# Kernel optimization log

Measured on AMD Instinct MI355X. Metric: run time of the kernel, lower is better.

## Reference

```python
import jax, jax.numpy as jnp
import numpy as np

V, E, H, B, T1, T2 = 32000, 300, 300, 64, 48, 48


def _lstm_last(x, Wih, Whh, bih, bhh):
    # x: [T, B, in]; returns final hidden state h_T: [B, H] (PyTorch gate order i,f,g,o)
    h0 = jnp.zeros((x.shape[1], Whh.shape[1]), x.dtype)
    def step(carry, xt):
        h, c = carry
        g = xt @ Wih.T + h @ Whh.T + bih + bhh
        i, f, gc, o = jnp.split(g, 4, axis=-1)
        c = jax.nn.sigmoid(f) * c + jax.nn.sigmoid(i) * jnp.tanh(gc)
        h = jax.nn.sigmoid(o) * jnp.tanh(c)
        return (h, c), None
    (h, _), _ = jax.lax.scan(step, (h0, h0), x)
    return h


def _bilstm_last(x, pf, pr):
    hf = _lstm_last(x, *pf)
    hr = _lstm_last(x[::-1], *pr)
    # faithful quirk: original reverses projr[0] along dim 0 == BATCH dim
    return jnp.concatenate([hf, hr[::-1]], axis=1)  # [B, 2H]


def _forward(x1, x2, x1_mask, x2_mask,
             emb, eW, eU, ebi, ebh, rW, rU, rbi, rbh,
             dW, dU, dbi, dbh, sW, sU, sbi, sbh,
             f1w, f1b, f2w, f2b, fow, fob):
    emb1 = emb[x1]  # [T1,B,E]
    emb2 = emb[x2]
    # encoder outputs final hidden [B,2H], broadcast over time by mask multiply (faithful quirk)
    ctx1 = _bilstm_last(emb1, (eW, eU, ebi, ebh), (rW, rU, rbi, rbh))[None] * x1_mask[:, :, None]  # [T1,B,2H]
    ctx2 = _bilstm_last(emb2, (eW, eU, ebi, ebh), (rW, rU, rbi, rbh))[None] * x2_mask[:, :, None]  # [T2,B,2H]
    c1 = ctx1.transpose(1, 0, 2)  # [B,T1,2H]
    c2 = ctx2.transpose(1, 0, 2)  # [B,T2,2H]
    # scores[b,i,j] = max_d c1[b,i,d]*c2[b,j,d]  (vectorized form of the O(T1*T2) python loop)
    scores = jnp.max(c1[:, :, None, :] * c2[:, None, :, :], axis=-1)  # [B,T1,T2]
    m1 = x1_mask.T  # [B,T1]
    m2 = x2_mask.T  # [B,T2]
    # masked softmax over hypothesis axis (axis=2)
    ea = jnp.exp(scores - jnp.max(scores, axis=2, keepdims=True)) * m2[:, None, :]
    alpha = ea / jnp.sum(ea, axis=2, keepdims=True)  # [B,T1,T2]
    # faithful quirk: MAX (not sum) pooling of attention-weighted hypothesis
    a_tilde = jnp.max(alpha[:, :, :, None] * c2[:, None, :, :], axis=2)  # [B,T1,2H]
    # masked softmax over premise axis (axis=1)
    eb = jnp.exp(scores - jnp.max(scores, axis=1, keepdims=True)) * m1[:, :, None]
    beta = eb / jnp.sum(eb, axis=1, keepdims=True)  # [B,T1,T2]
    b_tilde = jnp.einsum('bij,bid->bjd', beta, c1)  # [B,T2,2H]
    ctx1_ = a_tilde.transpose(1, 0, 2)  # [T1,B,2H]
    ctx2_ = b_tilde.transpose(1, 0, 2)  # [T2,B,2H]
    inp1 = jnp.concatenate([ctx1, ctx1_, ctx1 * ctx1_, ctx1 - ctx1_], axis=2)  # [T1,B,8H]
    inp2 = jnp.concatenate([ctx2, ctx2_, ctx2 * ctx2_, ctx2 - ctx2_], axis=2)
    h1 = jax.nn.relu(inp1 @ f1w.T + f1b)
    h2 = jax.nn.relu(inp2 @ f1w.T + f1b)
    ctx3 = _bilstm_last(h1, (dW, dU, dbi, dbh), (sW, sU, sbi, sbh))  # [B,2H]
    ctx4 = _bilstm_last(h2, (dW, dU, dbi, dbh), (sW, sU, sbi, sbh))  # [B,2H]
    w3 = ctx3[None] * x1_mask[:, :, None]  # [T1,B,2H]
    w4 = ctx4[None] * x2_mask[:, :, None]  # [T2,B,2H]
    logit = jnp.concatenate([
        w3.sum(0) / x1_mask.sum(0)[:, None], w3.max(0),
        w4.sum(0) / x2_mask.sum(0)[:, None], w4.max(0)], axis=1)  # [B,8H]
    logit = jnp.tanh(logit @ f2w.T + f2b)
    return logit @ fow.T + fob  # [B,3]


def setup_inputs() -> dict:
    key = jax.random.key(0)
    ks = jax.random.split(key, 32)
    s = 0.05
    n = lambda k, shape: jax.random.normal(k, shape, jnp.float32) * s
    d = {
        'x1': jax.random.randint(ks[0], (T1, B), 0, V, dtype=jnp.int32),
        'x1_mask': jnp.ones((T1, B), jnp.float32),
        'x2': jax.random.randint(ks[1], (T2, B), 0, V, dtype=jnp.int32),
        'x2_mask': jnp.ones((T2, B), jnp.float32),
        'l': T1,
        'embed_table': n(ks[2], (V, E)),
        'enc_Wih': n(ks[3], (4 * H, E)), 'enc_Whh': n(ks[4], (4 * H, H)),
        'enc_bih': n(ks[5], (4 * H,)), 'enc_bhh': n(ks[6], (4 * H,)),
        'encr_Wih': n(ks[7], (4 * H, E)), 'encr_Whh': n(ks[8], (4 * H, H)),
        'encr_bih': n(ks[9], (4 * H,)), 'encr_bhh': n(ks[10], (4 * H,)),
        'dec_Wih': n(ks[11], (4 * H, H)), 'dec_Whh': n(ks[12], (4 * H, H)),
        'dec_bih': n(ks[13], (4 * H,)), 'dec_bhh': n(ks[14], (4 * H,)),
        'decr_Wih': n(ks[15], (4 * H, H)), 'decr_Whh': n(ks[16], (4 * H, H)),
        'decr_bih': n(ks[17], (4 * H,)), 'decr_bhh': n(ks[18], (4 * H,)),
        'fc1_w': n(ks[19], (H, 8 * H)), 'fc1_b': n(ks[20], (H,)),
        'fc2_w': n(ks[21], (H, 8 * H)), 'fc2_b': n(ks[22], (H,)),
        'fco_w': n(ks[23], (3, H)), 'fco_b': n(ks[24], (3,)),
    }
    return d


def reference(x1, x1_mask, x2, x2_mask, l, embed_table,
              enc_Wih, enc_Whh, enc_bih, enc_bhh,
              encr_Wih, encr_Whh, encr_bih, encr_bhh,
              dec_Wih, dec_Whh, dec_bih, dec_bhh,
              decr_Wih, decr_Whh, decr_bih, decr_bhh,
              fc1_w, fc1_b, fc2_w, fc2_b, fco_w, fco_b):
    del l  # unused in original forward
    return _forward(x1, x2, x1_mask, x2_mask, embed_table,
                    enc_Wih, enc_Whh, enc_bih, enc_bhh,
                    encr_Wih, encr_Whh, encr_bih, encr_bhh,
                    dec_Wih, dec_Whh, dec_bih, dec_bhh,
                    decr_Wih, decr_Whh, decr_bih, decr_bhh,
                    fc1_w, fc1_b, fc2_w, fc2_b, fco_w, fco_b)
```

## Files before the change

kernel.cpp:

```cpp
#include <hip/hip_runtime.h>
#include <math.h>

typedef unsigned short u16;
typedef unsigned int u32;
typedef unsigned long long u64;
typedef __attribute__((ext_vector_type(8))) __bf16 bf16x8;
typedef __attribute__((ext_vector_type(4))) float f32x4;
typedef __attribute__((ext_vector_type(4))) _Float16 f16x4;

#define MR   6144
#define KP1  320
#define NPG  1280
#define NG   1200
#define WSEG 409600
#define UPSEG 409600
#define GT_H 163840

#define OFF_ABF    0UL
#define OFF_WBF    3932160UL
#define OFF_WCF    10485760UL
#define OFF_BIAS   12645760UL
#define OFF_GF     12664960UL
#define OFF_GR     28393600UL
#define OFF_HB     44122240UL
#define OFF_ENC    44286080UL
#define OFF_VB     44593280UL
#define OFF_CO     45822080UL
#define OFF_ATT    46436480UL
#define OFF_PT     46473344UL
#define OFF_LG     47087744UL
#define OFF_UP     47164544UL

#define HX_BYTES   655360UL

__device__ __forceinline__ float sigf(float x) { return 1.0f / (1.0f + expf(-x)); }
__device__ __forceinline__ float fsig(float x) { return 1.0f / (1.0f + __expf(-x)); }
__device__ __forceinline__ float ftanh(float x) { return 1.0f - 2.0f / (__expf(2.0f * x) + 1.0f); }

__device__ __forceinline__ u16 f2bf(float x) {
    union { float f; u32 u; } v; v.f = x;
    u32 r = v.u + 0x7fffu + ((v.u >> 16) & 1u);
    return (u16)(r >> 16);
}
__device__ __forceinline__ float bf2f(u16 x) {
    union { u32 u; float f; } v; v.u = ((u32)x) << 16; return v.f;
}

__device__ __forceinline__ void gld_lds16(const u16* g, u16* l) {
    __builtin_amdgcn_global_load_lds(
        (const __attribute__((address_space(1))) unsigned int*)g,
        (__attribute__((address_space(3))) unsigned int*)l, 16, 0, 0);
}

__global__ __launch_bounds__(256) void gather_bf(const int* __restrict__ x1,
                                                 const int* __restrict__ x2,
                                                 const float* __restrict__ emb,
                                                 u16* __restrict__ abf) {
    int idx = blockIdx.x * 256 + threadIdx.x;
    if (idx >= MR * KP1) return;
    int r = idx / KP1, k = idx % KP1;
    float v = 0.0f;
    if (k < 300) {
        int t = r >> 7, bc = r & 127;
        int tok = (bc < 64) ? x1[t * 64 + bc] : x2[t * 64 + bc - 64];
        v = emb[tok * 300 + k];
    }
    abf[idx] = f2bf(v);
}

__global__ __launch_bounds__(256) void wconv8_k(const float* __restrict__ w0, const float* __restrict__ w1,
                                                const float* __restrict__ w2, const float* __restrict__ w3,
                                                const float* __restrict__ w4, const float* __restrict__ w5,
                                                const float* __restrict__ w6, const float* __restrict__ w7,
                                                u16* __restrict__ out) {
    int idx = blockIdx.x * 256 + threadIdx.x;
    if (idx >= 8 * NPG * KP1) return;
    int s = idx / (NPG * KP1), rem = idx % (NPG * KP1);
    int r = rem / KP1, k = rem % KP1;
    const float* w = (s == 0) ? w0 : (s == 1) ? w1 : (s == 2) ? w2 : (s == 3) ? w3
                   : (s == 4) ? w4 : (s == 5) ? w5 : (s == 6) ? w6 : w7;
    float v = 0.0f;
    if (r < NG && k < 300) {
        int j = r >> 2, g = r & 3;
        v = w[(g * 300 + j) * 300 + k];
    }
    out[idx] = f2bf(v);
}

__global__ __launch_bounds__(256) void uperm_k(const u16* __restrict__ WU,
                                               u16* __restrict__ UP) {
    int idx = blockIdx.x * 256 + threadIdx.x;
    if (idx >= 4 * UPSEG) return;
    int seg = idx / UPSEG, pos = idx % UPSEG;
    int T = pos / 5120, kt = (pos / 512) % 10, l = (pos >> 3) & 63, e = pos & 7;
    int n = T * 16 + (l & 15);
    int k = kt * 32 + (l >> 4) * 8 + e;
    UP[idx] = WU[(size_t)seg * WSEG + (size_t)n * KP1 + k];
}

__global__ __launch_bounds__(256) void bconv_k(const float* __restrict__ b0i, const float* __restrict__ b0h,
                                               const float* __restrict__ b1i, const float* __restrict__ b1h,
                                               const float* __restrict__ b2i, const float* __restrict__ b2h,
                                               const float* __restrict__ b3i, const float* __restrict__ b3h,
                                               float* __restrict__ out) {
    int idx = blockIdx.x * 256 + threadIdx.x;
    if (idx >= 4 * NG) return;
    int s = idx / NG, n = idx % NG;
    int j = n >> 2, g = n & 3;
    int src = g * 300 + j;
    const float* bi = (s == 0) ? b0i : (s == 1) ? b1i : (s == 2) ? b2i : b3i;
    const float* bh = (s == 0) ? b0h : (s == 1) ? b1h : (s == 2) ? b2h : b3h;
    out[idx] = bi[src] + bh[src];
}

__global__ __launch_bounds__(256) void wcat_k(const float* __restrict__ f1w,
                                              float* __restrict__ wc) {
    int idx = blockIdx.x * 256 + threadIdx.x;
    if (idx >= 300 * 1800) return;
    int n = idx / 1800, k = idx % 1800;
    int nk = n * 2400 + k;
    float v;
    if (k < 600)       v = f1w[nk] + f1w[nk + 1800];
    else if (k < 1200) v = f1w[nk] - f1w[nk + 1200];
    else               v = f1w[nk];
    wc[idx] = v;
}

__global__ __launch_bounds__(256) void gemm_bt(const u16* __restrict__ A,
                                               const u16* __restrict__ B,
                                               const float* __restrict__ bias,
                                               _Float16* __restrict__ Gh) {
    __shared__ __align__(16) u16 smA[128 * 32];
    __shared__ __align__(16) u16 smB[128 * 32];
    int m0 = blockIdx.x * 128, n0 = blockIdx.y * 128;
    int tid = threadIdx.x, ln = tid & 63;
    int wm = (tid >> 6) & 1, wn = tid >> 7;
    int lrow = ln & 15, lq = ln >> 4;
    f32x4 acc[4][4] = {};
    for (int k0 = 0; k0 < KP1; k0 += 32) {
#pragma unroll
        for (int p = 0; p < 2; p++) {
            int e = (p * 256 + tid) * 8;
            int r = e >> 5, kk = e & 31;
            gld_lds16(A + (size_t)(m0 + r) * KP1 + k0 + kk, smA + e);
            gld_lds16(B + (size_t)(n0 + r) * KP1 + k0 + kk, smB + e);
        }
        __syncthreads();
        bf16x8 av[4], bv[4];
#pragma unroll
        for (int i = 0; i < 4; i++) {
            av[i] = *(const bf16x8*)&smA[(wm * 64 + i * 16 + lrow) * 32 + lq * 8];
            bv[i] = *(const bf16x8*)&smB[(wn * 64 + i * 16 + lrow) * 32 + lq * 8];
        }
#pragma unroll
        for (int i = 0; i < 4; i++)
#pragma unroll
            for (int j = 0; j < 4; j++)
                acc[i][j] = __builtin_amdgcn_mfma_f32_16x16x32_bf16(av[i], bv[j], acc[i][j], 0, 0, 0);
        __syncthreads();
    }
    size_t tb = (size_t)blockIdx.x * GT_H + (size_t)blockIdx.y * 16384
              + (size_t)wm * 8192 + (size_t)wn * 2048 + (size_t)ln * 4;
#pragma unroll
    for (int i = 0; i < 4; i++)
#pragma unroll
        for (int j = 0; j < 4; j++) {
            int n = n0 + wn * 64 + j * 16 + lrow;
            f16x4 v;
            if (n < NG) {
                float bb = bias[n];
#pragma unroll
                for (int r = 0; r < 4; r++) v[r] = (_Float16)(acc[i][j][r] + bb);
            } else {
                v = (f16x4)0;
            }
            *(f16x4*)(Gh + tb + (size_t)(i >> 1) * 4096 + (size_t)(((i & 1) * 4 + j)) * 256) = v;
        }
}

__global__ __launch_bounds__(256, 1) void lstm_sync(const _Float16* __restrict__ Gf,
                                                    const _Float16* __restrict__ Gr,
                                                    const u16* __restrict__ Upf,
                                                    const u16* __restrict__ Upr,
                                                    u64* __restrict__ hx,
                                                    u16* __restrict__ hb) {
    int nt = blockIdx.x, dir = blockIdx.y, half = blockIdx.z;
    const _Float16* G = dir ? Gr : Gf;
    const u16* Up = dir ? Upr : Upf;

    int tid = threadIdx.x, ln = tid & 63, w = tid >> 6;
    int wm = w & 1, wn = w >> 1;
    int lrow = ln & 15, lq = ln >> 4;

    __shared__ __align__(16) u16 Ulds[80 * 512];
    __shared__ __align__(16) u32 Hst[64 * 160];
    __shared__ float P[64][132];

    for (int p = 0; p < 20; p++) {
        int e = (p * 256 + tid) * 8;
        gld_lds16(Up + (size_t)nt * 40960 + e, Ulds + e);
    }
    __syncthreads();

    u32* HOw = (u32*)hb;

    int jp = tid & 15, bg = tid >> 4;
    float c[4][2];
#pragma unroll
    for (int q = 0; q < 4; q++) { c[q][0] = 0.0f; c[q][1] = 0.0f; }

    const _Float16* Gs = G + (size_t)nt * 16384 + (size_t)half * 8192
                       + (size_t)wm * 4096 + (size_t)wn * 2048 + (size_t)ln * 4;
    f16x4 gpre[8];
    {
        int ttg = dir ? 47 : 0;
        const _Float16* Gt = Gs + (size_t)ttg * GT_H;
#pragma unroll
        for (int f = 0; f < 8; f++) gpre[f] = *(const f16x4*)(Gt + (size_t)f * 256);
    }

    for (int t = 0; t < 48; t++) {
        {
            const u64* slab = hx + ((size_t)(t & 1) * 2 + dir) * 20480 + (size_t)half * 10240;
            u32 want = (u32)t;
            u32 hv[40];
            for (;;) {
                bool ok = true;
#pragma unroll
                for (int q = 0; q < 40; q++) {
                    u64 x = __hip_atomic_load(slab + q * 256 + tid,
                                              __ATOMIC_RELAXED, __HIP_MEMORY_SCOPE_AGENT);
                    hv[q] = (u32)x;
                    ok &= ((u32)(x >> 32) == want);
                }
                if (ok) break;
                __builtin_amdgcn_s_sleep(1);
            }
#pragma unroll
            for (int q = 0; q < 40; q++) {
                int idx = q * 256 + tid;
                int row = idx / 160, cc = idx - row * 160;
                Hst[row * 160 + (cc ^ ((row & 7) << 2))] = hv[q];
            }
        }
        __syncthreads();

        f32x4 acc[2][4];
#pragma unroll
        for (int i = 0; i < 2; i++)
#pragma unroll
            for (int j = 0; j < 4; j++) {
                f32x4 a;
#pragma unroll
                for (int r = 0; r < 4; r++) a[r] = (float)gpre[i * 4 + j][r];
                acc[i][j] = a;
            }

#pragma unroll
        for (int kt = 0; kt < 10; kt++) {
            bf16x8 av[2], bv[4];
#pragma unroll
            for (int i = 0; i < 2; i++) {
                int row = wm * 32 + i * 16 + lrow;
                int cc = (kt * 16 + lq * 4) ^ ((row & 7) << 2);
                av[i] = *(const bf16x8*)&Hst[row * 160 + cc];
            }
#pragma unroll
            for (int j = 0; j < 4; j++)
                bv[j] = *(const bf16x8*)&Ulds[((size_t)(wn * 4 + j) * 10 + kt) * 512 + ln * 8];
#pragma unroll
            for (int i = 0; i < 2; i++)
#pragma unroll
                for (int j = 0; j < 4; j++)
                    acc[i][j] = __builtin_amdgcn_mfma_f32_16x16x32_bf16(av[i], bv[j], acc[i][j], 0, 0, 0);
        }

#pragma unroll
        for (int i = 0; i < 2; i++)
#pragma unroll
            for (int j = 0; j < 4; j++) {
                int col = wn * 64 + j * 16 + lrow;
#pragma unroll
                for (int r = 0; r < 4; r++)
                    P[wm * 32 + i * 16 + lq * 4 + r][col] = acc[i][j][r];
            }
        __syncthreads();

        if (t < 47) {
            int ttg = dir ? 46 - t : t + 1;
            const _Float16* Gt = Gs + (size_t)ttg * GT_H;
#pragma unroll
            for (int f = 0; f < 8; f++) gpre[f] = *(const f16x4*)(Gt + (size_t)f * 256);
        }

        {
            u64* hxo = hx + ((size_t)((t + 1) & 1) * 2 + dir) * 20480;
            u64 tagb = ((u64)(u32)(t + 1)) << 32;
#pragma unroll
            for (int q = 0; q < 4; q++) {
                int bc = bg * 4 + q;
                f32x4 g0 = *(const f32x4*)&P[bc][8 * jp];
                f32x4 g1 = *(const f32x4*)&P[bc][8 * jp + 4];
                float cn0 = fsig(g0[1]) * c[q][0] + fsig(g0[0]) * ftanh(g0[2]);
                float hn0 = fsig(g0[3]) * ftanh(cn0);
                float cn1 = fsig(g1[1]) * c[q][1] + fsig(g1[0]) * ftanh(g1[2]);
                float hn1 = fsig(g1[3]) * ftanh(cn1);
                c[q][0] = cn0; c[q][1] = cn1;
                u32 pk = (u32)f2bf(hn0) | ((u32)f2bf(hn1) << 16);
                int bcg = half * 64 + bc;
                size_t oi = (size_t)bcg * 160 + nt * 16 + jp;
                if (t < 47)
                    __hip_atomic_store(hxo + oi, (u64)pk | tagb,
                                       __ATOMIC_RELAXED, __HIP_MEMORY_SCOPE_AGENT);
                else
                    HOw[(size_t)dir * 20480 + oi] = pk;
            }
        }
        __syncthreads();
    }
}

__global__ __launch_bounds__(256) void enc_k(const u16* __restrict__ hF,
                                             const u16* __restrict__ hR,
                                             float* __restrict__ enc) {
    int idx = blockIdx.x * 256 + threadIdx.x;
    if (idx >= 128 * 600) return;
    int bc = idx / 600, d = idx % 600;
    int seq = bc >> 6, b = bc & 63;
    enc[idx] = (d < 300) ? bf2f(hF[bc * KP1 + d])
                         : bf2f(hR[(seq * 64 + 63 - b) * KP1 + d - 300]);
}

__global__ __launch_bounds__(256) void vbuf_k(const float* __restrict__ enc,
                                              float* __restrict__ V) {
    int idx = blockIdx.x * 256 + threadIdx.x;
    if (idx >= 64 * 600) return;
    int b = idx / 600, d = idx % 600;
    float e1 = enc[b * 600 + d], e2 = enc[(64 + b) * 600 + d];
    float p = fmaxf(e2, 0.0f), nn = fminf(e2, 0.0f);
    V[0 * 38400 + idx] = e1;
    V[1 * 38400 + idx] = p;
    V[2 * 38400 + idx] = nn;
    V[3 * 38400 + idx] = e1 * p;
    V[4 * 38400 + idx] = e1 * nn;
    V[5 * 38400 + idx] = e2;
    V[6 * 38400 + idx] = e1;
    V[7 * 38400 + idx] = e1 * e2;
}

__global__ __launch_bounds__(256) void attn_lite(const float* __restrict__ enc,
                                                 const float* __restrict__ x1m,
                                                 const float* __restrict__ x2m,
                                                 float* __restrict__ AMX,
                                                 float* __restrict__ AMN,
                                                 float* __restrict__ SS) {
    int b = blockIdx.x, tid = threadIdx.x;
    __shared__ float sc[48][49];
    __shared__ float rmx[4], rmn[4];
    __shared__ float MxMn[2];
    float mx = -3.4e38f, mn = 3.4e38f;
    for (int d = tid; d < 600; d += 256) {
        float p = enc[b * 600 + d] * enc[(64 + b) * 600 + d];
        mx = fmaxf(mx, p); mn = fminf(mn, p);
    }
    for (int off = 32; off; off >>= 1) {
        mx = fmaxf(mx, __shfl_down(mx, off));
        mn = fminf(mn, __shfl_down(mn, off));
    }
    if ((tid & 63) == 0) { rmx[tid >> 6] = mx; rmn[tid >> 6] = mn; }
    __syncthreads();
    if (tid == 0) {
        MxMn[0] = fmaxf(fmaxf(rmx[0], rmx[1]), fmaxf(rmx[2], rmx[3]));
        MxMn[1] = fminf(fminf(rmn[0], rmn[1]), fminf(rmn[2], rmn[3]));
    }
    __syncthreads();
    float Mx = MxMn[0], Mn = MxMn[1];
    for (int idx = tid; idx < 2304; idx += 256) {
        int i = idx / 48, j = idx % 48;
        float q = x1m[i * 64 + b] * x2m[j * 64 + b];
        sc[i][j] = (q > 0.0f) ? q * Mx : ((q < 0.0f) ? q * Mn : 0.0f);
    }
    __syncthreads();
    if (tid < 48) {
        int i = tid;
        float m = -3.4e38f;
        for (int j = 0; j < 48; j++) m = fmaxf(m, sc[i][j]);
        float sum = 0.0f;
        for (int j = 0; j < 48; j++) sum += expf(sc[i][j] - m) * x2m[j * 64 + b];
        float wmax = -3.4e38f, wmin = 3.4e38f;
        for (int j = 0; j < 48; j++) {
            float w = expf(sc[i][j] - m) * x2m[j * 64 + b] * x2m[j * 64 + b];
            wmax = fmaxf(wmax, w); wmin = fminf(wmin, w);
        }
        AMX[i * 64 + b] = wmax / sum;
        AMN[i * 64 + b] = wmin / sum;
    } else if (tid >= 64 && tid < 112) {
        int j = tid - 64;
        float m = -3.4e38f;
        for (int i = 0; i < 48; i++) m = fmaxf(m, sc[i][j]);
        float sum = 0.0f, sm = 0.0f;
        for (int i = 0; i < 48; i++) {
            float e = expf(sc[i][j] - m) * x1m[i * 64 + b];
            sum += e; sm += e * x1m[i * 64 + b];
        }
        SS[j * 64 + b] = sm / sum;
    }
}

__global__ __launch_bounds__(256) void coeff_gemm(const float* __restrict__ V,
                                                  const float* __restrict__ Wc,
                                                  float* __restrict__ CO) {
    __shared__ float As[16][64];
    __shared__ float Ws[16][64];
    int s = blockIdx.y;
    const int offs[8] = {0, 600, 600, 1200, 1200, 0, 600, 1200};
    int koff = offs[s];
    const float* A = V + (size_t)s * 38400;
    float* C = CO + (size_t)s * 19200;
    int n0 = blockIdx.x * 64;
    int tid = threadIdx.x;
    int lrow = tid >> 2;
    int lk4 = (tid & 3) << 2;
    int tm = (tid & 15) << 2;
    int tn = (tid >> 4) << 2;
    int nW = n0 + lrow;
    float acc[4][4] = {};
    for (int k0 = 0; k0 < 600; k0 += 16) {
        __syncthreads();
#pragma unroll
        for (int q = 0; q < 4; q++) {
            int k = k0 + lk4 + q;
            As[lk4 + q][lrow] = (k < 600) ? A[lrow * 600 + k] : 0.0f;
            Ws[lk4 + q][lrow] = (k < 600 && nW < 300) ? Wc[(size_t)nW * 1800 + koff + k] : 0.0f;
        }
        __syncthreads();
#pragma unroll
        for (int kk = 0; kk < 16; kk++) {
            float a0 = As[kk][tm], a1 = As[kk][tm + 1], a2 = As[kk][tm + 2], a3 = As[kk][tm + 3];
            float w0 = Ws[kk][tn], w1 = Ws[kk][tn + 1], w2 = Ws[kk][tn + 2], w3 = Ws[kk][tn + 3];
            acc[0][0] += a0 * w0; acc[0][1] += a0 * w1; acc[0][2] += a0 * w2; acc[0][3] += a0 * w3;
            acc[1][0] += a1 * w0; acc[1][1] += a1 * w1; acc[1][2] += a1 * w2; acc[1][3] += a1 * w3;
            acc[2][0] += a2 * w0; acc[2][1] += a2 * w1; acc[2][2] += a2 * w2; acc[2][3] += a2 * w3;
            acc[3][0] += a3 * w0; acc[3][1] += a3 * w1; acc[3][2] += a3 * w2; acc[3][3] += a3 * w3;
        }
    }
#pragma unroll
    for (int ii = 0; ii < 4; ii++) {
        int m = tm + ii;
#pragma unroll
        for (int jn = 0; jn < 4; jn++) {
            int n = n0 + tn + jn;
            if (n < 300) C[m * 300 + n] = acc[ii][jn];
        }
    }
}

__global__ __launch_bounds__(320) void combine_k(const float* __restrict__ CO,
                                                 const float* __restrict__ f1b,
                                                 const float* __restrict__ x1m,
                                                 const float* __restrict__ x2m,
                                                 const float* __restrict__ AMX,
                                                 const float* __restrict__ AMN,
                                                 const float* __restrict__ SS,
                                                 u16* __restrict__ OUT) {
    int r = blockIdx.x;
    int t = r >> 7, bc = r & 127;
    int seq = bc >> 6, b = bc & 63;
    int n = threadIdx.x;
    if (n >= 300) return;
    int bn = b * 300 + n;
    float pre;
    if (seq == 0) {
        float m1 = x1m[t * 64 + b], am = AMX[t * 64 + b], an = AMN[t * 64 + b];
        pre = m1 * CO[bn] + am * CO[19200 + bn] + an * CO[2 * 19200 + bn]
            + m1 * am * CO[3 * 19200 + bn] + m1 * an * CO[4 * 19200 + bn] + f1b[n];
    } else {
        float m2 = x2m[t * 64 + b], sv = SS[t * 64 + b];
        pre = m2 * CO[5 * 19200 + bn] + sv * CO[6 * 19200 + bn]
            + m2 * sv * CO[7 * 19200 + bn] + f1b[n];
    }
    OUT[(size_t)r * KP1 + n] = f2bf(fmaxf(pre, 0.0f));
}

__global__ __launch_bounds__(256) void pool_k(const float* __restrict__ dctx,
                                              const float* __restrict__ x1m,
                                              const float* __restrict__ x2m,
                                              float* __restrict__ pooledT) {
    int idx = blockIdx.x * 256 + threadIdx.x;
    if (idx >= 64 * 2400) return;
    int b = idx / 2400, col = idx % 2400;
    int sec = col / 600, d = col % 600;
    const float* msk = (sec < 2) ? x1m : x2m;
    float v = dctx[((sec < 2 ? 0 : 64) + b) * 600 + d];
    float out;
    if ((sec & 1) == 0) {
        float s = 0, sm = 0;
        for (int t = 0; t < 48; t++) { float mv = msk[t * 64 + b]; s += v * mv; sm += mv; }
        out = s / sm;
    } else {
        float m = -3.4e38f;
        for (int t = 0; t < 48; t++) m = fmaxf(m, v * msk[t * 64 + b]);
        out = m;
    }
    pooledT[col * 64 + b] = out;
}

__global__ __launch_bounds__(256) void fc2_k2(const float* __restrict__ pooledT,
                                              const float* __restrict__ f2w,
                                              const float* __restrict__ f2b,
                                              float* __restrict__ logit) {
    __shared__ float wl[2400];
    __shared__ float red[256];
    int n = blockIdx.x;
    for (int i = threadIdx.x; i < 2400; i += 256) wl[i] = f2w[n * 2400 + i];
    __syncthreads();
    int b = threadIdx.x & 63, kc = threadIdx.x >> 6;
    float acc = 0.0f;
    int k0 = kc * 600;
    for (int kk = 0; kk < 600; kk++) acc += pooledT[(k0 + kk) * 64 + b] * wl[k0 + kk];
    red[threadIdx.x] = acc;
    __syncthreads();
    if (threadIdx.x < 64) {
        float s = red[b] + red[64 + b] + red[128 + b] + red[192 + b];
        logit[b * 300 + n] = tanhf(s + f2b[n]);
    }
}

__global__ __launch_bounds__(64) void out_k2(const float* __restrict__ logit,
                                             const float* __restrict__ fow,
                                             const float* __restrict__ fob,
                                             float* __restrict__ out) {
    int b = blockIdx.x, tid = threadIdx.x;
    float p0 = 0, p1 = 0, p2 = 0;
    for (int k = tid; k < 300; k += 64) {
        float l = logit[b * 300 + k];
        p0 += l * fow[k]; p1 += l * fow[300 + k]; p2 += l * fow[600 + k];
    }
    for (int off = 32; off; off >>= 1) {
        p0 += __shfl_down(p0, off);
        p1 += __shfl_down(p1, off);
        p2 += __shfl_down(p2, off);
    }
    if (tid == 0) {
        out[b * 3 + 0] = p0 + fob[0];
        out[b * 3 + 1] = p1 + fob[1];
        out[b * 3 + 2] = p2 + fob[2];
    }
}

extern "C" void kernel_launch(void* const* d_in, const int* in_sizes, int n_in,
                              void* d_out, int out_size, void* d_ws, size_t ws_size,
                              hipStream_t stream) {
    (void)in_sizes; (void)n_in; (void)out_size; (void)ws_size;
    const int*   x1  = (const int*)d_in[0];
    const float* x1m = (const float*)d_in[1];
    const int*   x2  = (const int*)d_in[2];
    const float* x2m = (const float*)d_in[3];
    const float* emb = (const float*)d_in[5];
    const float* eW  = (const float*)d_in[6];
    const float* eU  = (const float*)d_in[7];
    const float* ebi = (const float*)d_in[8];
    const float* ebh = (const float*)d_in[9];
    const float* rW  = (const float*)d_in[10];
    const float* rU  = (const float*)d_in[11];
    const float* rbi = (const float*)d_in[12];
    const float* rbh = (const float*)d_in[13];
    const float* dW  = (const float*)d_in[14];
    const float* dU  = (const float*)d_in[15];
    const float* dbi = (const float*)d_in[16];
    const float* dbh = (const float*)d_in[17];
    const float* sW  = (const float*)d_in[18];
    const float* sU  = (const float*)d_in[19];
    const float* sbi = (const float*)d_in[20];
    const float* sbh = (const float*)d_in[21];
    const float* f1w = (const float*)d_in[22];
    const float* f1b = (const float*)d_in[23];
    const float* f2w = (const float*)d_in[24];
    const float* f2b = (const float*)d_in[25];
    const float* fow = (const float*)d_in[26];
    const float* fob = (const float*)d_in[27];

    char* wsb = (char*)d_ws;
    u16*       ABF  = (u16*)(wsb + OFF_ABF);
    u16*       WBF  = (u16*)(wsb + OFF_WBF);
    float*     WCF  = (float*)(wsb + OFF_WCF);
    float*     BIAS = (float*)(wsb + OFF_BIAS);
    _Float16*  GFh  = (_Float16*)(wsb + OFF_GF);
    _Float16*  GRh  = (_Float16*)(wsb + OFF_GR);
    u16*       HB   = (u16*)(wsb + OFF_HB);
    float*     ENC  = (float*)(wsb + OFF_ENC);
    float*     VB   = (float*)(wsb + OFF_VB);
    float*     CO   = (float*)(wsb + OFF_CO);
    float*     AMX  = (float*)(wsb + OFF_ATT);
    float*     AMN  = AMX + 3072;
    float*     SS   = AMX + 6144;
    float*     PT   = (float*)(wsb + OFF_PT);
    float*     LG   = (float*)(wsb + OFF_LG);
    u16*       UP   = (u16*)(wsb + OFF_UP);
    u64*       HX64 = (u64*)(wsb + OFF_ABF);

    u16* HF0 = HB;
    u16* HR0 = HB + 40960;

    gather_bf<<<dim3((MR * KP1 + 255) / 256), 256, 0, stream>>>(x1, x2, emb, ABF);
    wconv8_k<<<dim3((8 * NPG * KP1 + 255) / 256), 256, 0, stream>>>(eW, rW, dW, sW, eU, rU, dU, sU, WBF);
    uperm_k<<<dim3((4 * UPSEG + 255) / 256), 256, 0, stream>>>(WBF + 4 * WSEG, UP);
    bconv_k<<<dim3((4 * NG + 255) / 256), 256, 0, stream>>>(ebi, ebh, rbi, rbh, dbi, dbh, sbi, sbh, BIAS);
    wcat_k<<<dim3((300 * 1800 + 255) / 256), 256, 0, stream>>>(f1w, WCF);

    gemm_bt<<<dim3(48, 10), 256, 0, stream>>>(ABF, WBF,        BIAS,      GFh);
    gemm_bt<<<dim3(48, 10), 256, 0, stream>>>(ABF, WBF + WSEG, BIAS + NG, GRh);
    hipMemsetAsync(wsb + OFF_ABF, 0, HX_BYTES, stream);
    lstm_sync<<<dim3(10, 2, 2), 256, 0, stream>>>(GFh, GRh, UP, UP + UPSEG, HX64, HB);

    enc_k<<<dim3((128 * 600 + 255) / 256), 256, 0, stream>>>(HF0, HR0, ENC);
    vbuf_k<<<dim3((64 * 600 + 255) / 256), 256, 0, stream>>>(ENC, VB);
    attn_lite<<<dim3(64), 256, 0, stream>>>(ENC, x1m, x2m, AMX, AMN, SS);
    coeff_gemm<<<dim3(5, 8), 256, 0, stream>>>(VB, WCF, CO);
    combine_k<<<dim3(6144), 320, 0, stream>>>(CO, f1b, x1m, x2m, AMX, AMN, SS, ABF);

    gemm_bt<<<dim3(48, 10), 256, 0, stream>>>(ABF, WBF + 2 * WSEG, BIAS + 2 * NG, GFh);
    gemm_bt<<<dim3(48, 10), 256, 0, stream>>>(ABF, WBF + 3 * WSEG, BIAS + 3 * NG, GRh);
    hipMemsetAsync(wsb + OFF_ABF, 0, HX_BYTES, stream);
    lstm_sync<<<dim3(10, 2, 2), 256, 0, stream>>>(GFh, GRh, UP + 2 * UPSEG, UP + 3 * UPSEG, HX64, HB);

    enc_k<<<dim3((128 * 600 + 255) / 256), 256, 0, stream>>>(HF0, HR0, ENC);
    pool_k<<<dim3((64 * 2400 + 255) / 256), 256, 0, stream>>>(ENC, x1m, x2m, PT);
    fc2_k2<<<dim3(300), 256, 0, stream>>>(PT, f2w, f2b, LG);
    out_k2<<<dim3(64), 64, 0, stream>>>(LG, fow, fob, (float*)d_out);
}
```

Before: 889.7 us.

## Fuse prep kernels, batch paired GEMMs, and relax LSTM polling and sync

The five weight/embedding preparation kernels become one block-partitioned prep kernel, and the recurrent weights are permuted straight from fp32 instead of through an intermediate bf16 copy. The forward and reverse input-projection GEMMs are merged into a single launch using a z grid dimension. In the persistent LSTM loop, the spin-wait now re-polls only the slab entries that have not yet arrived, the trailing __syncthreads is dropped, and the next-step gate prefetch moves after the hidden-state publish. This cuts launch count and per-step latency, but dropping the barrier relies on the later barrier inside the loop to keep shared-memory reuse safe.

```diff
diff --git a/kernel.cpp b/kernel.cpp
--- a/kernel.cpp
+++ b/kernel.cpp
@@ -33,7 +33,6 @@
 
 #define HX_BYTES   655360UL
 
-__device__ __forceinline__ float sigf(float x) { return 1.0f / (1.0f + expf(-x)); }
 __device__ __forceinline__ float fsig(float x) { return 1.0f / (1.0f + __expf(-x)); }
 __device__ __forceinline__ float ftanh(float x) { return 1.0f - 2.0f / (__expf(2.0f * x) + 1.0f); }
 
@@ -52,86 +51,94 @@
         (__attribute__((address_space(3))) unsigned int*)l, 16, 0, 0);
 }
 
-__global__ __launch_bounds__(256) void gather_bf(const int* __restrict__ x1,
-                                                 const int* __restrict__ x2,
-                                                 const float* __restrict__ emb,
-                                                 u16* __restrict__ abf) {
-    int idx = blockIdx.x * 256 + threadIdx.x;
-    if (idx >= MR * KP1) return;
-    int r = idx / KP1, k = idx % KP1;
-    float v = 0.0f;
-    if (k < 300) {
-        int t = r >> 7, bc = r & 127;
-        int tok = (bc < 64) ? x1[t * 64 + bc] : x2[t * 64 + bc - 64];
-        v = emb[tok * 300 + k];
-    }
-    abf[idx] = f2bf(v);
-}
-
-__global__ __launch_bounds__(256) void wconv8_k(const float* __restrict__ w0, const float* __restrict__ w1,
-                                                const float* __restrict__ w2, const float* __restrict__ w3,
-                                                const float* __restrict__ w4, const float* __restrict__ w5,
-                                                const float* __restrict__ w6, const float* __restrict__ w7,
-                                                u16* __restrict__ out) {
-    int idx = blockIdx.x * 256 + threadIdx.x;
-    if (idx >= 8 * NPG * KP1) return;
-    int s = idx / (NPG * KP1), rem = idx % (NPG * KP1);
-    int r = rem / KP1, k = rem % KP1;
-    const float* w = (s == 0) ? w0 : (s == 1) ? w1 : (s == 2) ? w2 : (s == 3) ? w3
-                   : (s == 4) ? w4 : (s == 5) ? w5 : (s == 6) ? w6 : w7;
-    float v = 0.0f;
-    if (r < NG && k < 300) {
-        int j = r >> 2, g = r & 3;
-        v = w[(g * 300 + j) * 300 + k];
-    }
-    out[idx] = f2bf(v);
-}
-
-__global__ __launch_bounds__(256) void uperm_k(const u16* __restrict__ WU,
-                                               u16* __restrict__ UP) {
-    int idx = blockIdx.x * 256 + threadIdx.x;
-    if (idx >= 4 * UPSEG) return;
-    int seg = idx / UPSEG, pos = idx % UPSEG;
-    int T = pos / 5120, kt = (pos / 512) % 10, l = (pos >> 3) & 63, e = pos & 7;
-    int n = T * 16 + (l & 15);
-    int k = kt * 32 + (l >> 4) * 8 + e;
-    UP[idx] = WU[(size_t)seg * WSEG + (size_t)n * KP1 + k];
-}
-
-__global__ __launch_bounds__(256) void bconv_k(const float* __restrict__ b0i, const float* __restrict__ b0h,
-                                               const float* __restrict__ b1i, const float* __restrict__ b1h,
-                                               const float* __restrict__ b2i, const float* __restrict__ b2h,
-                                               const float* __restrict__ b3i, const float* __restrict__ b3h,
-                                               float* __restrict__ out) {
-    int idx = blockIdx.x * 256 + threadIdx.x;
-    if (idx >= 4 * NG) return;
-    int s = idx / NG, n = idx % NG;
-    int j = n >> 2, g = n & 3;
-    int src = g * 300 + j;
-    const float* bi = (s == 0) ? b0i : (s == 1) ? b1i : (s == 2) ? b2i : b3i;
-    const float* bh = (s == 0) ? b0h : (s == 1) ? b1h : (s == 2) ? b2h : b3h;
-    out[idx] = bi[src] + bh[src];
-}
-
-__global__ __launch_bounds__(256) void wcat_k(const float* __restrict__ f1w,
-                                              float* __restrict__ wc) {
-    int idx = blockIdx.x * 256 + threadIdx.x;
-    if (idx >= 300 * 1800) return;
-    int n = idx / 1800, k = idx % 1800;
-    int nk = n * 2400 + k;
-    float v;
-    if (k < 600)       v = f1w[nk] + f1w[nk + 1800];
-    else if (k < 1200) v = f1w[nk] - f1w[nk + 1200];
-    else               v = f1w[nk];
-    wc[idx] = v;
+#define PREP_B0 7680
+#define PREP_B1 14080
+#define PREP_B2 20480
+#define PREP_B3 20499
+#define PREP_B4 22609
+__global__ __launch_bounds__(256) void prep_k(
+    const int* __restrict__ x1, const int* __restrict__ x2, const float* __restrict__ emb,
+    const float* __restrict__ w0, const float* __restrict__ w1,
+    const float* __restrict__ w2, const float* __restrict__ w3,
+    const float* __restrict__ u0, const float* __restrict__ u1,
+    const float* __restrict__ u2, const float* __restrict__ u3,
+    const float* __restrict__ b0i, const float* __restrict__ b0h,
+    const float* __restrict__ b1i, const float* __restrict__ b1h,
+    const float* __restrict__ b2i, const float* __restrict__ b2h,
+    const float* __restrict__ b3i, const float* __restrict__ b3h,
+    const float* __restrict__ f1w,
+    u16* __restrict__ abf, u16* __restrict__ wbf, u16* __restrict__ up,
+    float* __restrict__ bias, float* __restrict__ wc) {
+    int bid = blockIdx.x;
+    if (bid < PREP_B0) {
+        int idx = bid * 256 + threadIdx.x;
+        int r = idx / KP1, k = idx % KP1;
+        float v = 0.0f;
+        if (k < 300) {
+            int t = r >> 7, bc = r & 127;
+            int tok = (bc < 64) ? x1[t * 64 + bc] : x2[t * 64 + bc - 64];
+            v = emb[tok * 300 + k];
+        }
+        abf[idx] = f2bf(v);
+    } else if (bid < PREP_B1) {
+        int idx = (bid - PREP_B0) * 256 + threadIdx.x;
+        int s = idx / (NPG * KP1), rem = idx % (NPG * KP1);
+        int r = rem / KP1, k = rem % KP1;
+        const float* w = (s == 0) ? w0 : (s == 1) ? w1 : (s == 2) ? w2 : w3;
+        float v = 0.0f;
+        if (r < NG && k < 300) {
+            int j = r >> 2, g = r & 3;
+            v = w[(g * 300 + j) * 300 + k];
+        }
+        wbf[idx] = f2bf(v);
+    } else if (bid < PREP_B2) {
+        int idx = (bid - PREP_B1) * 256 + threadIdx.x;
+        int seg = idx / UPSEG, pos = idx % UPSEG;
+        int T = pos / 5120, kt = (pos / 512) % 10, l = (pos >> 3) & 63, e = pos & 7;
+        int n = T * 16 + (l & 15);
+        int k = kt * 32 + (l >> 4) * 8 + e;
+        const float* us = (seg == 0) ? u0 : (seg == 1) ? u1 : (seg == 2) ? u2 : u3;
+        float v = 0.0f;
+        if (n < NG && k < 300) {
+            int j = n >> 2, g = n & 3;
+            v = us[(g * 300 + j) * 300 + k];
+        }
+        up[idx] = f2bf(v);
+    } else if (bid < PREP_B3) {
+        int idx = (bid - PREP_B2) * 256 + threadIdx.x;
+        if (idx < 4 * NG) {
+            int s = idx / NG, n = idx % NG;
+            int j = n >> 2, g = n & 3;
+            int src = g * 300 + j;
+            const float* bi = (s == 0) ? b0i : (s == 1) ? b1i : (s == 2) ? b2i : b3i;
+            const float* bh = (s == 0) ? b0h : (s == 1) ? b1h : (s == 2) ? b2h : b3h;
+            bias[idx] = bi[src] + bh[src];
+        }
+    } else {
+        int idx = (bid - PREP_B3) * 256 + threadIdx.x;
+        if (idx < 300 * 1800) {
+            int n = idx / 1800, k = idx % 1800;
+            int nk = n * 2400 + k;
+            float v;
+            if (k < 600)       v = f1w[nk] + f1w[nk + 1800];
+            else if (k < 1200) v = f1w[nk] - f1w[nk + 1200];
+            else               v = f1w[nk];
+            wc[idx] = v;
+        }
+    }
 }
 
 __global__ __launch_bounds__(256) void gemm_bt(const u16* __restrict__ A,
-                                               const u16* __restrict__ B,
-                                               const float* __restrict__ bias,
-                                               _Float16* __restrict__ Gh) {
+                                               const u16* __restrict__ Wb,
+                                               const float* __restrict__ biasb,
+                                               _Float16* __restrict__ G0,
+                                               _Float16* __restrict__ G1) {
     __shared__ __align__(16) u16 smA[128 * 32];
     __shared__ __align__(16) u16 smB[128 * 32];
+    int sidx = blockIdx.z;
+    const u16* B = Wb + (size_t)sidx * WSEG;
+    const float* bias = biasb + sidx * NG;
+    _Float16* Gh = sidx ? G1 : G0;
     int m0 = blockIdx.x * 128, n0 = blockIdx.y * 128;
     int tid = threadIdx.x, ln = tid & 63;
     int wm = (tid >> 6) & 1, wn = tid >> 7;
@@ -224,17 +231,24 @@
             const u64* slab = hx + ((size_t)(t & 1) * 2 + dir) * 20480 + (size_t)half * 10240;
             u32 want = (u32)t;
             u32 hv[40];
-            for (;;) {
-                bool ok = true;
+            u64 miss = 0;
+#pragma unroll
+            for (int q = 0; q < 40; q++) {
+                u64 x = __hip_atomic_load(slab + q * 256 + tid,
+                                          __ATOMIC_RELAXED, __HIP_MEMORY_SCOPE_AGENT);
+                hv[q] = (u32)x;
+                miss |= ((u64)((u32)(x >> 32) != want)) << q;
+            }
+            while (miss) {
+                __builtin_amdgcn_s_sleep(1);
 #pragma unroll
                 for (int q = 0; q < 40; q++) {
-                    u64 x = __hip_atomic_load(slab + q * 256 + tid,
-                                              __ATOMIC_RELAXED, __HIP_MEMORY_SCOPE_AGENT);
-                    hv[q] = (u32)x;
-                    ok &= ((u32)(x >> 32) == want);
+                    if (miss & (1ull << q)) {
+                        u64 x = __hip_atomic_load(slab + q * 256 + tid,
+                                                  __ATOMIC_RELAXED, __HIP_MEMORY_SCOPE_AGENT);
+                        if ((u32)(x >> 32) == want) { hv[q] = (u32)x; miss &= ~(1ull << q); }
+                    }
                 }
-                if (ok) break;
-                __builtin_amdgcn_s_sleep(1);
             }
 #pragma unroll
             for (int q = 0; q < 40; q++) {
@@ -285,13 +299,6 @@
                     P[wm * 32 + i * 16 + lq * 4 + r][col] = acc[i][j][r];
             }
         __syncthreads();
-
-        if (t < 47) {
-            int ttg = dir ? 46 - t : t + 1;
-            const _Float16* Gt = Gs + (size_t)ttg * GT_H;
-#pragma unroll
-            for (int f = 0; f < 8; f++) gpre[f] = *(const f16x4*)(Gt + (size_t)f * 256);
-        }
 
         {
             u64* hxo = hx + ((size_t)((t + 1) & 1) * 2 + dir) * 20480;
@@ -316,7 +323,13 @@
                     HOw[(size_t)dir * 20480 + oi] = pk;
             }
         }
-        __syncthreads();
+
+        if (t < 47) {
+            int ttg = dir ? 46 - t : t + 1;
+            const _Float16* Gt = Gs + (size_t)ttg * GT_H;
+#pragma unroll
+            for (int f = 0; f < 8; f++) gpre[f] = *(const f16x4*)(Gt + (size_t)f * 256);
+        }
     }
 }
 
@@ -602,14 +615,12 @@
     u16* HF0 = HB;
     u16* HR0 = HB + 40960;
 
-    gather_bf<<<dim3((MR * KP1 + 255) / 256), 256, 0, stream>>>(x1, x2, emb, ABF);
-    wconv8_k<<<dim3((8 * NPG * KP1 + 255) / 256), 256, 0, stream>>>(eW, rW, dW, sW, eU, rU, dU, sU, WBF);
-    uperm_k<<<dim3((4 * UPSEG + 255) / 256), 256, 0, stream>>>(WBF + 4 * WSEG, UP);
-    bconv_k<<<dim3((4 * NG + 255) / 256), 256, 0, stream>>>(ebi, ebh, rbi, rbh, dbi, dbh, sbi, sbh, BIAS);
-    wcat_k<<<dim3((300 * 1800 + 255) / 256), 256, 0, stream>>>(f1w, WCF);
-
-    gemm_bt<<<dim3(48, 10), 256, 0, stream>>>(ABF, WBF,        BIAS,      GFh);
-    gemm_bt<<<dim3(48, 10), 256, 0, stream>>>(ABF, WBF + WSEG, BIAS + NG, GRh);
+    prep_k<<<dim3(PREP_B4), 256, 0, stream>>>(
+        x1, x2, emb, eW, rW, dW, sW, eU, rU, dU, sU,
+        ebi, ebh, rbi, rbh, dbi, dbh, sbi, sbh, f1w,
+        ABF, WBF, UP, BIAS, WCF);
+
+    gemm_bt<<<dim3(48, 10, 2), 256, 0, stream>>>(ABF, WBF, BIAS, GFh, GRh);
     hipMemsetAsync(wsb + OFF_ABF, 0, HX_BYTES, stream);
     lstm_sync<<<dim3(10, 2, 2), 256, 0, stream>>>(GFh, GRh, UP, UP + UPSEG, HX64, HB);
 
@@ -619,8 +630,7 @@
     coeff_gemm<<<dim3(5, 8), 256, 0, stream>>>(VB, WCF, CO);
     combine_k<<<dim3(6144), 320, 0, stream>>>(CO, f1b, x1m, x2m, AMX, AMN, SS, ABF);
 
-    gemm_bt<<<dim3(48, 10), 256, 0, stream>>>(ABF, WBF + 2 * WSEG, BIAS + 2 * NG, GFh);
-    gemm_bt<<<dim3(48, 10), 256, 0, stream>>>(ABF, WBF + 3 * WSEG, BIAS + 3 * NG, GRh);
+    gemm_bt<<<dim3(48, 10, 2), 256, 0, stream>>>(ABF, WBF + 2 * WSEG, BIAS + 2 * NG, GFh, GRh);
     hipMemsetAsync(wsb + OFF_ABF, 0, HX_BYTES, stream);
     lstm_sync<<<dim3(10, 2, 2), 256, 0, stream>>>(GFh, GRh, UP + 2 * UPSEG, UP + 3 * UPSEG, HX64, HB);
 
```

Measured after the change: 1.349 ms. 51.7% more time.
